# Optimization experiments

Hardware: AMD Instinct MI355X
Metric: run time of the kernel (lower is better)

The kernel has to match this reference:

```python
import jax, jax.numpy as jnp
import numpy as np

V = 4096          # vocab size (blank = V-1)
BLANK = V - 1
D = 512           # encoder dim
J = 640           # joint dim
E = 512           # embedding dim
H = 640           # prediction-net LSTM hidden
T = 8192          # frames


def setup_inputs() -> dict:
    key = jax.random.key(0)
    ks = jax.random.split(key, 12)
    s = lambda *sh: 1.0 / np.sqrt(sh[0])
    return {
        "enc_out": jax.random.normal(ks[0], (1, T, D), jnp.float32),
        "embed":   jax.random.normal(ks[1], (V, E), jnp.float32) * 0.02,
        "Wx":      jax.random.normal(ks[2], (E, 4 * H), jnp.float32) * s(E),
        "Wh":      jax.random.normal(ks[3], (H, 4 * H), jnp.float32) * s(H),
        "b_lstm":  jnp.zeros((4 * H,), jnp.float32),
        "Wdp":     jax.random.normal(ks[4], (H, J), jnp.float32) * s(H),
        "bdp":     jnp.zeros((J,), jnp.float32),
        "Wenc":    jax.random.normal(ks[5], (D, J), jnp.float32) * s(D),
        "benc":    jnp.zeros((J,), jnp.float32),
        "Wout":    jax.random.normal(ks[6], (J, V), jnp.float32) * s(J),
        "bout":    jnp.zeros((V,), jnp.float32),
    }


def _pred_step(tok, h, c, embed, Wx, Wh, b_lstm, Wdp, bdp):
    # single-token LSTM prediction-network step + output projection (decoder.pred)
    e = embed[tok]                                    # [E]
    g = e @ Wx + h @ Wh + b_lstm                      # [4H]
    i, f, gg, o = jnp.split(g, 4)
    c2 = jax.nn.sigmoid(f) * c + jax.nn.sigmoid(i) * jnp.tanh(gg)
    h2 = jax.nn.sigmoid(o) * jnp.tanh(c2)
    dp = h2 @ Wdp + bdp                               # [J] dec projection
    return dp, h2, c2


def reference(enc_out, embed, Wx, Wh, b_lstm, Wdp, bdp, Wenc, benc, Wout, bout):
    # decoder.enc_proj: [1,T,D] -> [T,J]
    enc_proj = enc_out[0] @ Wenc + benc

    # initial pred step fed with the blank token, zero hidden state
    dp0, h0, c0 = _pred_step(BLANK, jnp.zeros((H,), enc_out.dtype),
                             jnp.zeros((H,), enc_out.dtype),
                             embed, Wx, Wh, b_lstm, Wdp, bdp)

    def step(carry, enc_f):
        dp, h, c = carry
        # decoder.joint(enc, dec) = Wout @ tanh(enc_proj + dec_proj), then log_softmax
        logits = jnp.tanh(enc_f + dp) @ Wout + bout   # [V]
        logp = jax.nn.log_softmax(logits, axis=-1)
        tok = jnp.argmax(logp, axis=-1)
        dp2, h2, c2 = _pred_step(tok, h, c, embed, Wx, Wh, b_lstm, Wdp, bdp)
        nb = tok != BLANK                             # advance pred net only on emission
        carry = (jnp.where(nb, dp2, dp), jnp.where(nb, h2, h), jnp.where(nb, c2, c))
        return carry, logp

    _, logps = jax.lax.scan(step, (dp0, h0, c0), enc_proj)  # logps: [T, V]
    return logps
```

## Files before the change

kernel.cpp:

```cpp
#include <hip/hip_runtime.h>
#include <stdint.h>

#define T_FRAMES 8192
#define DIM_D 512
#define DIM_J 640
#define DIM_E 512
#define DIM_H 640
#define DIM_V 4096
#define G4H   2560
#define TOK_BLANK 4095
#define NBLK 256
#define NTHR 256

#define WS_HW   0
#define WS_DW   (WS_HW + 640*8)
#define WS_SA   (WS_DW + 640*8)
#define WS_SB   (WS_SA + 256*8)
#define WS_SC   (WS_SB + 256*8)
#define WS_BAR  (WS_SC + 256*8)

__device__ __forceinline__ float sigm(float x) { return 1.f / (1.f + __expf(-x)); }

__device__ __forceinline__ void st64(unsigned long long* p, unsigned tag, unsigned pay) {
  __hip_atomic_store(p, ((unsigned long long)tag << 32) | (unsigned long long)pay,
                     __ATOMIC_RELAXED, __HIP_MEMORY_SCOPE_AGENT);
}
__device__ __forceinline__ unsigned long long ld64(const unsigned long long* p) {
  return __hip_atomic_load(p, __ATOMIC_RELAXED, __HIP_MEMORY_SCOPE_AGENT);
}
__device__ __forceinline__ bool tagok(unsigned long long w, unsigned tag) {
  return (int)((unsigned)(w >> 32) - tag) >= 0;
}

__device__ __forceinline__ void gbar_init(unsigned* flags, int bid, int tid) {
  __syncthreads();
  if (tid == 0)
    __hip_atomic_store(&flags[bid * 16], 1u, __ATOMIC_RELEASE, __HIP_MEMORY_SCOPE_AGENT);
  unsigned f;
  do { f = __hip_atomic_load(&flags[tid * 16], __ATOMIC_RELAXED, __HIP_MEMORY_SCOPE_AGENT); }
  while ((int)(f - 1u) < 0);
  __builtin_amdgcn_fence(__ATOMIC_ACQUIRE, "agent");
  __syncthreads();
}

extern "C" __global__ void __launch_bounds__(NTHR, 1)
rnnt_greedy2(const float* __restrict__ enc,
             const float* __restrict__ embed,
             const float* __restrict__ Wx,
             const float* __restrict__ Wh,
             const float* __restrict__ b_lstm,
             const float* __restrict__ Wdp,
             const float* __restrict__ bdp,
             const float* __restrict__ Wenc,
             const float* __restrict__ benc,
             const float* __restrict__ Wout,
             const float* __restrict__ bout,
             float* __restrict__ out,
             unsigned long long* __restrict__ hw,
             unsigned long long* __restrict__ dw,
             unsigned long long* __restrict__ sA,
             unsigned long long* __restrict__ sB,
             unsigned long long* __restrict__ sC,
             unsigned* __restrict__ barflag)
{
  __shared__ float smem[29792];

  const int tid  = threadIdx.x;
  const int bid  = blockIdx.x;
  const int wid  = tid >> 6;
  const int lane = tid & 63;

  float* woutl = smem;
  float* wxl   = smem + 10240;
  float* whl   = smem + 16384;
  float* wdpl  = smem + 24064;
  float* h_com = smem + 25984;
  float* h2_l  = smem + 26624;
  float* dp_com= smem + 27264;
  float* x_l   = smem + 27904;
  float* enc_l = smem + 28544;
  float* ebuf  = smem + 29184;
  float* logit_l = smem + 29696;
  float* g_l     = smem + 29712;
  float* c_l     = smem + 29724;
  float* bout_l  = smem + 29728;
  float* blst_l  = smem + 29744;
  float* bdp_l   = smem + 29756;
  float* red     = smem + 29760;
  float* enc_lds = smem;

  const int h0 = (bid * 5) >> 1;
  const int h1 = ((bid + 1) * 5) >> 1;
  const int nH = h1 - h0;
  const int ncols = nH * 4;
  const int vb = bid << 4;

  {
    const int r0 = bid * 32;
    const float4* src = (const float4*)(enc + (size_t)r0 * DIM_D);
    float4* dst = (float4*)enc_lds;
    for (int i = tid; i < 32 * DIM_D / 4; i += NTHR) dst[i] = src[i];
    __syncthreads();
    for (int jj = tid; jj < DIM_J; jj += NTHR) {
      float acc[32];
      #pragma unroll
      for (int r = 0; r < 32; ++r) acc[r] = 0.f;
      for (int k = 0; k < DIM_D; ++k) {
        float w = Wenc[(size_t)k * DIM_J + jj];
        #pragma unroll
        for (int r = 0; r < 32; ++r) acc[r] += enc_lds[r * DIM_D + k] * w;
      }
      float bj = benc[jj];
      for (int r = 0; r < 32; ++r) out[(size_t)(r0 + r) * DIM_V + jj] = acc[r] + bj;
    }
    __syncthreads();
  }

  for (int idx = tid; idx < 16 * DIM_J; idx += NTHR) {
    int vl = idx / DIM_J, j = idx - vl * DIM_J;
    woutl[idx] = Wout[(size_t)j * DIM_V + vb + vl];
  }
  for (int idx = tid; idx < ncols * DIM_E; idx += NTHR) {
    int c = idx >> 9, k = idx & 511;
    int gcol = (c & 3) * DIM_H + h0 + (c >> 2);
    wxl[idx] = Wx[(size_t)k * G4H + gcol];
  }
  for (int idx = tid; idx < ncols * DIM_H; idx += NTHR) {
    int c = idx / DIM_H, k = idx - c * DIM_H;
    int gcol = (c & 3) * DIM_H + h0 + (c >> 2);
    whl[idx] = Wh[(size_t)k * G4H + gcol];
  }
  for (int idx = tid; idx < nH * DIM_H; idx += NTHR) {
    int jl = idx / DIM_H, k = idx - jl * DIM_H;
    wdpl[idx] = Wdp[(size_t)k * DIM_J + h0 + jl];
  }
  if (tid < 16) bout_l[tid] = bout[vb + tid];
  if (tid < ncols) blst_l[tid] = b_lstm[(tid & 3) * DIM_H + h0 + (tid >> 2)];
  if (tid < nH) bdp_l[tid] = bdp[h0 + tid];
  for (int i = tid; i < DIM_H; i += NTHR) h_com[i] = 0.f;
  if (tid < 4) c_l[tid] = 0.f;

  gbar_init(barflag, bid, tid);

  for (int t = -1; t < T_FRAMES; ++t) {
    const unsigned TAG = (unsigned)(t + 2);
    int tok; bool nb;

    if (t >= 0) {
      {
        const float* w0 = woutl + (wid * 4 + 0) * DIM_J;
        const float* w1 = woutl + (wid * 4 + 1) * DIM_J;
        const float* w2 = woutl + (wid * 4 + 2) * DIM_J;
        const float* w3 = woutl + (wid * 4 + 3) * DIM_J;
        float a0 = 0, a1 = 0, a2 = 0, a3 = 0;
        #pragma unroll
        for (int i = 0; i < 10; ++i) {
          int k = lane + (i << 6);
          float xv = x_l[k];
          a0 += xv * w0[k]; a1 += xv * w1[k]; a2 += xv * w2[k]; a3 += xv * w3[k];
        }
        #pragma unroll
        for (int m = 32; m; m >>= 1) {
          a0 += __shfl_xor(a0, m); a1 += __shfl_xor(a1, m);
          a2 += __shfl_xor(a2, m); a3 += __shfl_xor(a3, m);
        }
        if (lane == 0) {
          logit_l[wid * 4 + 0] = a0 + bout_l[wid * 4 + 0];
          logit_l[wid * 4 + 1] = a1 + bout_l[wid * 4 + 1];
          logit_l[wid * 4 + 2] = a2 + bout_l[wid * 4 + 2];
          logit_l[wid * 4 + 3] = a3 + bout_l[wid * 4 + 3];
        }
      }
      __syncthreads();

      {
        int prow = (t + 1 < T_FRAMES) ? t + 1 : t;
        if (tid >= 64 && tid < 224) {
          float4 ef = *(const float4*)(out + (size_t)prow * DIM_V + (tid - 64) * 4);
          *(float4*)(enc_l + (tid - 64) * 4) = ef;
        }
      }
      if (wid == 0) {
        float v  = (lane < 16) ? logit_l[lane] : -3.4e38f;
        int   vi = vb + (lane & 15);
        float m = v; int mi = vi;
        #pragma unroll
        for (int s = 32; s; s >>= 1) {
          float om = __shfl_xor(m, s); int oi = __shfl_xor(mi, s);
          if (om > m || (om == m && oi < mi)) { m = om; mi = oi; }
        }
        float e = (lane < 16) ? __expf(v - m) : 0.f;
        #pragma unroll
        for (int s = 32; s; s >>= 1) e += __shfl_xor(e, s);
        if (lane == 0) {
          st64(sA + bid, TAG, __float_as_uint(m));
          st64(sB + bid, TAG, __float_as_uint(e));
          st64(sC + bid, TAG, (unsigned)mi);
        }
      }

      unsigned long long wa = 0, wb = 0, wc = 0;
      {
        bool ra = false, rb = false, rc = false;
        while (!(ra && rb && rc)) {
          unsigned long long ta = wa, tb = wb, tc = wc;
          if (!ra) ta = ld64(sA + tid);
          if (!rb) tb = ld64(sB + tid);
          if (!rc) tc = ld64(sC + tid);
          if (!ra && tagok(ta, TAG)) { wa = ta; ra = true; }
          if (!rb && tagok(tb, TAG)) { wb = tb; rb = true; }
          if (!rc && tagok(tc, TAG)) { wc = tc; rc = true; }
          if (!(ra && rb && rc)) __builtin_amdgcn_s_sleep(1);
        }
      }
      const float mi0 = __uint_as_float((unsigned)wa);
      const float ei0 = __uint_as_float((unsigned)wb);
      const int   ii0 = (int)(unsigned)wc;
      float m = mi0; int idx = ii0;
      #pragma unroll
      for (int s = 32; s; s >>= 1) {
        float om = __shfl_xor(m, s); int oi = __shfl_xor(idx, s);
        if (om > m || (om == m && oi < idx)) { m = om; idx = oi; }
      }
      if (lane == 0) { red[wid] = m; ((int*)red)[4 + wid] = idx; }
      __syncthreads();
      float gm = red[0]; int gtok = ((int*)red)[4];
      #pragma unroll
      for (int w = 1; w < 4; ++w) {
        float om = red[w]; int oi = ((int*)red)[4 + w];
        if (om > gm || (om == gm && oi < gtok)) { gm = om; gtok = oi; }
      }
      float term = ei0 * __expf(mi0 - gm);
      #pragma unroll
      for (int s = 32; s; s >>= 1) term += __shfl_xor(term, s);
      if (lane == 0) red[8 + wid] = term;
      __syncthreads();
      const float lse = gm + __logf(red[8] + red[9] + red[10] + red[11]);

      if (tid < 16) out[(size_t)t * DIM_V + vb + tid] = logit_l[tid] - lse;

      tok = gtok;
      nb = (tok != TOK_BLANK);
      if (t == T_FRAMES - 1) break;
    } else {
      tok = TOK_BLANK;
      nb = true;
      if (tid >= 64 && tid < 224) {
        float4 ef = *(const float4*)(out + (size_t)(tid - 64) * 4);
        *(float4*)(enc_l + (tid - 64) * 4) = ef;
      }
    }

    if (tid < 128) {
      float4 ev = *(const float4*)(embed + (size_t)tok * DIM_E + tid * 4);
      *(float4*)(ebuf + tid * 4) = ev;
    }
    __syncthreads();
    for (int c = wid; c < ncols; c += 4) {
      const float* wx = wxl + c * DIM_E;
      const float* wh = whl + c * DIM_H;
      float acc = 0.f;
      #pragma unroll
      for (int i = 0; i < 8; ++i)  { int k = lane + (i << 6); acc += ebuf[k] * wx[k]; }
      #pragma unroll
      for (int i = 0; i < 10; ++i) { int k = lane + (i << 6); acc += h_com[k] * wh[k]; }
      #pragma unroll
      for (int s = 32; s; s >>= 1) acc += __shfl_xor(acc, s);
      if (lane == 0) g_l[c] = acc + blst_l[c];
    }
    __syncthreads();
    if (tid < nH) {
      float c_old = c_l[tid];
      float gi = g_l[tid * 4 + 0], gf = g_l[tid * 4 + 1];
      float gg = g_l[tid * 4 + 2], go_ = g_l[tid * 4 + 3];
      float c2  = sigm(gf) * c_old + sigm(gi) * tanhf(gg);
      float h2v = sigm(go_) * tanhf(c2);
      c_l[tid] = nb ? c2 : c_old;
      st64(hw + h0 + tid, TAG, __float_as_uint(h2v));
    }

    {
      const bool has2 = (tid < 128);
      unsigned long long w0 = 0, w1 = 0, w2 = 0;
      bool r0 = false, r1 = false, r2 = !has2;
      while (!(r0 && r1 && r2)) {
        unsigned long long t0 = w0, t1 = w1, t2 = w2;
        if (!r0) t0 = ld64(hw + tid);
        if (!r1) t1 = ld64(hw + tid + 256);
        if (!r2) t2 = ld64(hw + tid + 512);
        if (!r0 && tagok(t0, TAG)) { w0 = t0; r0 = true; }
        if (!r1 && tagok(t1, TAG)) { w1 = t1; r1 = true; }
        if (!r2 && tagok(t2, TAG)) { w2 = t2; r2 = true; }
        if (!(r0 && r1 && r2)) __builtin_amdgcn_s_sleep(1);
      }
      float h2a = __uint_as_float((unsigned)w0);
      float h2b = __uint_as_float((unsigned)w1);
      h2_l[tid] = h2a;        h_com[tid]       = nb ? h2a : h_com[tid];
      h2_l[tid + 256] = h2b;  h_com[tid + 256] = nb ? h2b : h_com[tid + 256];
      if (has2) {
        float h2c = __uint_as_float((unsigned)w2);
        h2_l[tid + 512] = h2c; h_com[tid + 512] = nb ? h2c : h_com[tid + 512];
      }
    }
    __syncthreads();

    if (wid < nH) {
      const float* wp = wdpl + wid * DIM_H;
      float acc = 0.f;
      #pragma unroll
      for (int i = 0; i < 10; ++i) { int k = lane + (i << 6); acc += h2_l[k] * wp[k]; }
      #pragma unroll
      for (int s = 32; s; s >>= 1) acc += __shfl_xor(acc, s);
      if (lane == 0) st64(dw + h0 + wid, TAG, __float_as_uint(acc + bdp_l[wid]));
    }

    {
      const bool has2 = (tid < 128);
      unsigned long long w0 = 0, w1 = 0, w2 = 0;
      bool r0 = false, r1 = false, r2 = !has2;
      while (!(r0 && r1 && r2)) {
        unsigned long long t0 = w0, t1 = w1, t2 = w2;
        if (!r0) t0 = ld64(dw + tid);
        if (!r1) t1 = ld64(dw + tid + 256);
        if (!r2) t2 = ld64(dw + tid + 512);
        if (!r0 && tagok(t0, TAG)) { w0 = t0; r0 = true; }
        if (!r1 && tagok(t1, TAG)) { w1 = t1; r1 = true; }
        if (!r2 && tagok(t2, TAG)) { w2 = t2; r2 = true; }
        if (!(r0 && r1 && r2)) __builtin_amdgcn_s_sleep(1);
      }
      float d0 = __uint_as_float((unsigned)w0);
      float d1 = __uint_as_float((unsigned)w1);
      float dn0 = nb ? d0 : dp_com[tid];
      float dn1 = nb ? d1 : dp_com[tid + 256];
      dp_com[tid] = dn0;       x_l[tid]       = tanhf(enc_l[tid] + dn0);
      dp_com[tid + 256] = dn1; x_l[tid + 256] = tanhf(enc_l[tid + 256] + dn1);
      if (has2) {
        float d2 = __uint_as_float((unsigned)w2);
        float dn2 = nb ? d2 : dp_com[tid + 512];
        dp_com[tid + 512] = dn2; x_l[tid + 512] = tanhf(enc_l[tid + 512] + dn2);
      }
    }
    __syncthreads();
  }
}

extern "C" void kernel_launch(void* const* d_in, const int* in_sizes, int n_in,
                              void* d_out, int out_size, void* d_ws, size_t ws_size,
                              hipStream_t stream) {
  const float* enc    = (const float*)d_in[0];
  const float* embed  = (const float*)d_in[1];
  const float* Wx     = (const float*)d_in[2];
  const float* Wh     = (const float*)d_in[3];
  const float* b_lstm = (const float*)d_in[4];
  const float* Wdp    = (const float*)d_in[5];
  const float* bdp    = (const float*)d_in[6];
  const float* Wenc   = (const float*)d_in[7];
  const float* benc   = (const float*)d_in[8];
  const float* Wout   = (const float*)d_in[9];
  const float* bout   = (const float*)d_in[10];
  float* out = (float*)d_out;
  char* ws = (char*)d_ws;
  unsigned long long* hw = (unsigned long long*)(ws + WS_HW);
  unsigned long long* dw = (unsigned long long*)(ws + WS_DW);
  unsigned long long* sA = (unsigned long long*)(ws + WS_SA);
  unsigned long long* sB = (unsigned long long*)(ws + WS_SB);
  unsigned long long* sC = (unsigned long long*)(ws + WS_SC);
  unsigned* barflag = (unsigned*)(ws + WS_BAR);

  hipLaunchKernelGGL(rnnt_greedy2, dim3(NBLK), dim3(NTHR), 0, stream,
                     enc, embed, Wx, Wh, b_lstm, Wdp, bdp, Wenc, benc, Wout, bout,
                     out, hw, dw, sA, sB, sC, barflag);
}
```

Before: 114.3 ms.

## Restructure per-frame cross-block exchange to cut global sync round-trips

Packs the per-block max and argmax into a single tagged 64-bit word and drops the third exchange array. The argmax is reduced by one wave so the token is known before the sum-exp exchange. The log-softmax normalisation moves off the critical path and overlaps the Wh part of the LSTM matvec, and each block now publishes tanh(enc+dp) directly instead of dp, so only one wave polls each exchange. The sum of exponentials is computed without subtracting the max, which risks overflow for large logits.

```diff
diff --git a/kernel.cpp b/kernel.cpp
--- a/kernel.cpp
+++ b/kernel.cpp
@@ -13,11 +13,10 @@
 #define NTHR 256
 
 #define WS_HW   0
-#define WS_DW   (WS_HW + 640*8)
-#define WS_SA   (WS_DW + 640*8)
+#define WS_XW   (WS_HW + 640*8)
+#define WS_SA   (WS_XW + 640*8)
 #define WS_SB   (WS_SA + 256*8)
-#define WS_SC   (WS_SB + 256*8)
-#define WS_BAR  (WS_SC + 256*8)
+#define WS_BAR  (WS_SB + 256*8)
 
 __device__ __forceinline__ float sigm(float x) { return 1.f / (1.f + __expf(-x)); }
 
@@ -30,6 +29,9 @@
 }
 __device__ __forceinline__ bool tagok(unsigned long long w, unsigned tag) {
   return (int)((unsigned)(w >> 32) - tag) >= 0;
+}
+__device__ __forceinline__ bool tagok16(unsigned long long w, unsigned tag16) {
+  return (short)((unsigned short)(w >> 48) - (unsigned short)tag16) >= 0;
 }
 
 __device__ __forceinline__ void gbar_init(unsigned* flags, int bid, int tid) {
@@ -44,7 +46,7 @@
 }
 
 extern "C" __global__ void __launch_bounds__(NTHR, 1)
-rnnt_greedy2(const float* __restrict__ enc,
+rnnt_greedy3(const float* __restrict__ enc,
              const float* __restrict__ embed,
              const float* __restrict__ Wx,
              const float* __restrict__ Wh,
@@ -57,13 +59,12 @@
              const float* __restrict__ bout,
              float* __restrict__ out,
              unsigned long long* __restrict__ hw,
-             unsigned long long* __restrict__ dw,
+             unsigned long long* __restrict__ xw,
              unsigned long long* __restrict__ sA,
              unsigned long long* __restrict__ sB,
-             unsigned long long* __restrict__ sC,
              unsigned* __restrict__ barflag)
 {
-  __shared__ float smem[29792];
+  __shared__ float smem[28512];
 
   const int tid  = threadIdx.x;
   const int bid  = blockIdx.x;
@@ -76,17 +77,16 @@
   float* wdpl  = smem + 24064;
   float* h_com = smem + 25984;
   float* h2_l  = smem + 26624;
-  float* dp_com= smem + 27264;
-  float* x_l   = smem + 27904;
-  float* enc_l = smem + 28544;
-  float* ebuf  = smem + 29184;
-  float* logit_l = smem + 29696;
-  float* g_l     = smem + 29712;
-  float* c_l     = smem + 29724;
-  float* bout_l  = smem + 29728;
-  float* blst_l  = smem + 29744;
-  float* bdp_l   = smem + 29756;
-  float* red     = smem + 29760;
+  float* x_l   = smem + 27264;
+  float* ebuf  = smem + 27904;
+  float* logit_l = smem + 28416;
+  float* g_l     = smem + 28432;
+  float* c_l     = smem + 28444;
+  float* dpc_l   = smem + 28448;
+  float* bout_l  = smem + 28452;
+  float* blst_l  = smem + 28468;
+  float* bdp_l   = smem + 28480;
+  float* red     = smem + 28484;
   float* enc_lds = smem;
 
   const int h0 = (bid * 5) >> 1;
@@ -142,10 +142,22 @@
 
   gbar_init(barflag, bid, tid);
 
+  const int  slot = (wid == 0) ? 0 : wid - 1;
+  const int  c0 = slot, c1 = slot + 3, c2 = slot + 6, c3 = slot + 9;
+  const bool v2 = (c2 < ncols), v3 = (c3 < ncols);
+  const bool lstmw = (wid != 1);
+
   for (int t = -1; t < T_FRAMES; ++t) {
     const unsigned TAG = (unsigned)(t + 2);
+    const bool last = (t == T_FRAMES - 1);
+
+    float encj = 0.f;
+    {
+      int prow = (t + 1 < T_FRAMES) ? (t + 1) : (T_FRAMES - 1);
+      if (wid < nH && lane == 0) encj = out[(size_t)prow * DIM_V + h0 + wid];
+    }
+
     int tok; bool nb;
-
     if (t >= 0) {
       {
         const float* w0 = woutl + (wid * 4 + 0) * DIM_J;
@@ -160,9 +172,9 @@
           a0 += xv * w0[k]; a1 += xv * w1[k]; a2 += xv * w2[k]; a3 += xv * w3[k];
         }
         #pragma unroll
-        for (int m = 32; m; m >>= 1) {
-          a0 += __shfl_xor(a0, m); a1 += __shfl_xor(a1, m);
-          a2 += __shfl_xor(a2, m); a3 += __shfl_xor(a3, m);
+        for (int s = 32; s; s >>= 1) {
+          a0 += __shfl_xor(a0, s); a1 += __shfl_xor(a1, s);
+          a2 += __shfl_xor(a2, s); a3 += __shfl_xor(a3, s);
         }
         if (lane == 0) {
           logit_l[wid * 4 + 0] = a0 + bout_l[wid * 4 + 0];
@@ -173,13 +185,6 @@
       }
       __syncthreads();
 
-      {
-        int prow = (t + 1 < T_FRAMES) ? t + 1 : t;
-        if (tid >= 64 && tid < 224) {
-          float4 ef = *(const float4*)(out + (size_t)prow * DIM_V + (tid - 64) * 4);
-          *(float4*)(enc_l + (tid - 64) * 4) = ef;
-        }
-      }
       if (wid == 0) {
         float v  = (lane < 16) ? logit_l[lane] : -3.4e38f;
         int   vi = vb + (lane & 15);
@@ -189,156 +194,171 @@
           float om = __shfl_xor(m, s); int oi = __shfl_xor(mi, s);
           if (om > m || (om == m && oi < mi)) { m = om; mi = oi; }
         }
-        float e = (lane < 16) ? __expf(v - m) : 0.f;
+        float e = (lane < 16) ? __expf(v) : 0.f;
         #pragma unroll
         for (int s = 32; s; s >>= 1) e += __shfl_xor(e, s);
         if (lane == 0) {
-          st64(sA + bid, TAG, __float_as_uint(m));
+          unsigned long long cw = ((unsigned long long)(TAG & 0xffffu) << 48)
+                                | ((unsigned long long)__float_as_uint(m) << 16)
+                                | (unsigned long long)(unsigned)(mi & 0xffff);
+          __hip_atomic_store(sA + bid, cw, __ATOMIC_RELAXED, __HIP_MEMORY_SCOPE_AGENT);
           st64(sB + bid, TAG, __float_as_uint(e));
-          st64(sC + bid, TAG, (unsigned)mi);
-        }
-      }
-
-      unsigned long long wa = 0, wb = 0, wc = 0;
-      {
-        bool ra = false, rb = false, rc = false;
-        while (!(ra && rb && rc)) {
-          unsigned long long ta = wa, tb = wb, tc = wc;
-          if (!ra) ta = ld64(sA + tid);
-          if (!rb) tb = ld64(sB + tid);
-          if (!rc) tc = ld64(sC + tid);
-          if (!ra && tagok(ta, TAG)) { wa = ta; ra = true; }
-          if (!rb && tagok(tb, TAG)) { wb = tb; rb = true; }
-          if (!rc && tagok(tc, TAG)) { wc = tc; rc = true; }
-          if (!(ra && rb && rc)) __builtin_amdgcn_s_sleep(1);
-        }
-      }
-      const float mi0 = __uint_as_float((unsigned)wa);
-      const float ei0 = __uint_as_float((unsigned)wb);
-      const int   ii0 = (int)(unsigned)wc;
-      float m = mi0; int idx = ii0;
+        }
+        unsigned long long cv0 = 0, cv1 = 0, cv2 = 0, cv3 = 0;
+        unsigned rdy = 0;
+        while (rdy != 0xfu) {
+          if (!(rdy & 1u)) { unsigned long long w = ld64(sA + lane);        if (tagok16(w, TAG)) { cv0 = w; rdy |= 1u; } }
+          if (!(rdy & 2u)) { unsigned long long w = ld64(sA + lane + 64);   if (tagok16(w, TAG)) { cv1 = w; rdy |= 2u; } }
+          if (!(rdy & 4u)) { unsigned long long w = ld64(sA + lane + 128);  if (tagok16(w, TAG)) { cv2 = w; rdy |= 4u; } }
+          if (!(rdy & 8u)) { unsigned long long w = ld64(sA + lane + 192);  if (tagok16(w, TAG)) { cv3 = w; rdy |= 8u; } }
+          if (rdy != 0xfu) __builtin_amdgcn_s_sleep(1);
+        }
+        float bm = -3.4e38f; int bi = 0x7fffffff;
+        {
+          float mm; int ii;
+          mm = __uint_as_float((unsigned)(cv0 >> 16)); ii = ((int)lane << 4)        | (int)(cv0 & 0xfu) | (int)((cv0 >> 4) & 0xff0u);
+          ii = (int)(cv0 & 0xffffu);
+          if (mm > bm || (mm == bm && ii < bi)) { bm = mm; bi = ii; }
+          mm = __uint_as_float((unsigned)(cv1 >> 16)); ii = (int)(cv1 & 0xffffu);
+          if (mm > bm || (mm == bm && ii < bi)) { bm = mm; bi = ii; }
+          mm = __uint_as_float((unsigned)(cv2 >> 16)); ii = (int)(cv2 & 0xffffu);
+          if (mm > bm || (mm == bm && ii < bi)) { bm = mm; bi = ii; }
+          mm = __uint_as_float((unsigned)(cv3 >> 16)); ii = (int)(cv3 & 0xffffu);
+          if (mm > bm || (mm == bm && ii < bi)) { bm = mm; bi = ii; }
+        }
+        #pragma unroll
+        for (int s = 32; s; s >>= 1) {
+          float om = __shfl_xor(bm, s); int oi = __shfl_xor(bi, s);
+          if (om > bm || (om == bm && oi < bi)) { bm = om; bi = oi; }
+        }
+        if (lane == 0) ((int*)red)[0] = bi;
+      }
+      __syncthreads();
+      tok = ((int*)red)[0];
+      nb = (tok != TOK_BLANK);
+    } else {
+      tok = TOK_BLANK; nb = true;
+    }
+
+    float4 ev;
+    if (wid >= 2 && !last) ev = *(const float4*)(embed + (size_t)tok * DIM_E + (tid - 128) * 4);
+    float acc0 = 0, acc1 = 0, acc2 = 0, acc3 = 0;
+    if (lstmw && !last) {
+      #pragma unroll
+      for (int i = 0; i < 10; ++i) {
+        int k = lane + (i << 6);
+        float hv = h_com[k];
+        acc0 += hv * whl[c0 * DIM_H + k];
+        acc1 += hv * whl[c1 * DIM_H + k];
+        if (v2) acc2 += hv * whl[c2 * DIM_H + k];
+        if (v3) acc3 += hv * whl[c3 * DIM_H + k];
+      }
+    }
+    if (wid == 1 && t >= 0) {
+      unsigned long long s0 = 0, s1 = 0, s2 = 0, s3 = 0;
+      unsigned rdy = 0;
+      while (rdy != 0xfu) {
+        if (!(rdy & 1u)) { unsigned long long w = ld64(sB + lane);        if (tagok(w, TAG)) { s0 = w; rdy |= 1u; } }
+        if (!(rdy & 2u)) { unsigned long long w = ld64(sB + lane + 64);   if (tagok(w, TAG)) { s1 = w; rdy |= 2u; } }
+        if (!(rdy & 4u)) { unsigned long long w = ld64(sB + lane + 128);  if (tagok(w, TAG)) { s2 = w; rdy |= 4u; } }
+        if (!(rdy & 8u)) { unsigned long long w = ld64(sB + lane + 192);  if (tagok(w, TAG)) { s3 = w; rdy |= 8u; } }
+        if (rdy != 0xfu) __builtin_amdgcn_s_sleep(1);
+      }
+      float s = __uint_as_float((unsigned)s0) + __uint_as_float((unsigned)s1)
+              + __uint_as_float((unsigned)s2) + __uint_as_float((unsigned)s3);
+      #pragma unroll
+      for (int sh = 32; sh; sh >>= 1) s += __shfl_xor(s, sh);
+      float lse = __logf(s);
+      if (lane < 16) out[(size_t)t * DIM_V + vb + lane] = logit_l[lane] - lse;
+    }
+    if (wid >= 2 && !last) *(float4*)(ebuf + (tid - 128) * 4) = ev;
+    __syncthreads();
+    if (last) break;
+
+    if (lstmw) {
+      #pragma unroll
+      for (int i = 0; i < 8; ++i) {
+        int k = lane + (i << 6);
+        float evv = ebuf[k];
+        acc0 += evv * wxl[c0 * DIM_E + k];
+        acc1 += evv * wxl[c1 * DIM_E + k];
+        if (v2) acc2 += evv * wxl[c2 * DIM_E + k];
+        if (v3) acc3 += evv * wxl[c3 * DIM_E + k];
+      }
       #pragma unroll
       for (int s = 32; s; s >>= 1) {
-        float om = __shfl_xor(m, s); int oi = __shfl_xor(idx, s);
-        if (om > m || (om == m && oi < idx)) { m = om; idx = oi; }
-      }
-      if (lane == 0) { red[wid] = m; ((int*)red)[4 + wid] = idx; }
-      __syncthreads();
-      float gm = red[0]; int gtok = ((int*)red)[4];
-      #pragma unroll
-      for (int w = 1; w < 4; ++w) {
-        float om = red[w]; int oi = ((int*)red)[4 + w];
-        if (om > gm || (om == gm && oi < gtok)) { gm = om; gtok = oi; }
-      }
-      float term = ei0 * __expf(mi0 - gm);
-      #pragma unroll
-      for (int s = 32; s; s >>= 1) term += __shfl_xor(term, s);
-      if (lane == 0) red[8 + wid] = term;
-      __syncthreads();
-      const float lse = gm + __logf(red[8] + red[9] + red[10] + red[11]);
-
-      if (tid < 16) out[(size_t)t * DIM_V + vb + tid] = logit_l[tid] - lse;
-
-      tok = gtok;
-      nb = (tok != TOK_BLANK);
-      if (t == T_FRAMES - 1) break;
-    } else {
-      tok = TOK_BLANK;
-      nb = true;
-      if (tid >= 64 && tid < 224) {
-        float4 ef = *(const float4*)(out + (size_t)(tid - 64) * 4);
-        *(float4*)(enc_l + (tid - 64) * 4) = ef;
-      }
-    }
-
-    if (tid < 128) {
-      float4 ev = *(const float4*)(embed + (size_t)tok * DIM_E + tid * 4);
-      *(float4*)(ebuf + tid * 4) = ev;
-    }
-    __syncthreads();
-    for (int c = wid; c < ncols; c += 4) {
-      const float* wx = wxl + c * DIM_E;
-      const float* wh = whl + c * DIM_H;
-      float acc = 0.f;
-      #pragma unroll
-      for (int i = 0; i < 8; ++i)  { int k = lane + (i << 6); acc += ebuf[k] * wx[k]; }
-      #pragma unroll
-      for (int i = 0; i < 10; ++i) { int k = lane + (i << 6); acc += h_com[k] * wh[k]; }
-      #pragma unroll
-      for (int s = 32; s; s >>= 1) acc += __shfl_xor(acc, s);
-      if (lane == 0) g_l[c] = acc + blst_l[c];
-    }
-    __syncthreads();
+        acc0 += __shfl_xor(acc0, s); acc1 += __shfl_xor(acc1, s);
+        acc2 += __shfl_xor(acc2, s); acc3 += __shfl_xor(acc3, s);
+      }
+      if (lane == 0) {
+        g_l[c0] = acc0 + blst_l[c0];
+        g_l[c1] = acc1 + blst_l[c1];
+        if (v2) g_l[c2] = acc2 + blst_l[c2];
+        if (v3) g_l[c3] = acc3 + blst_l[c3];
+      }
+    }
+    __syncthreads();
+
     if (tid < nH) {
       float c_old = c_l[tid];
       float gi = g_l[tid * 4 + 0], gf = g_l[tid * 4 + 1];
       float gg = g_l[tid * 4 + 2], go_ = g_l[tid * 4 + 3];
-      float c2  = sigm(gf) * c_old + sigm(gi) * tanhf(gg);
-      float h2v = sigm(go_) * tanhf(c2);
-      c_l[tid] = nb ? c2 : c_old;
+      float c2v = sigm(gf) * c_old + sigm(gi) * tanhf(gg);
+      float h2v = sigm(go_) * tanhf(c2v);
+      c_l[tid] = nb ? c2v : c_old;
       st64(hw + h0 + tid, TAG, __float_as_uint(h2v));
     }
-
-    {
-      const bool has2 = (tid < 128);
-      unsigned long long w0 = 0, w1 = 0, w2 = 0;
-      bool r0 = false, r1 = false, r2 = !has2;
-      while (!(r0 && r1 && r2)) {
-        unsigned long long t0 = w0, t1 = w1, t2 = w2;
-        if (!r0) t0 = ld64(hw + tid);
-        if (!r1) t1 = ld64(hw + tid + 256);
-        if (!r2) t2 = ld64(hw + tid + 512);
-        if (!r0 && tagok(t0, TAG)) { w0 = t0; r0 = true; }
-        if (!r1 && tagok(t1, TAG)) { w1 = t1; r1 = true; }
-        if (!r2 && tagok(t2, TAG)) { w2 = t2; r2 = true; }
-        if (!(r0 && r1 && r2)) __builtin_amdgcn_s_sleep(1);
-      }
-      float h2a = __uint_as_float((unsigned)w0);
-      float h2b = __uint_as_float((unsigned)w1);
-      h2_l[tid] = h2a;        h_com[tid]       = nb ? h2a : h_com[tid];
-      h2_l[tid + 256] = h2b;  h_com[tid + 256] = nb ? h2b : h_com[tid + 256];
-      if (has2) {
-        float h2c = __uint_as_float((unsigned)w2);
-        h2_l[tid + 512] = h2c; h_com[tid + 512] = nb ? h2c : h_com[tid + 512];
+    if (wid == 0) {
+      unsigned long long hv[10]; unsigned rdy = 0;
+      while (rdy != 0x3ffu) {
+        #pragma unroll
+        for (int i = 0; i < 10; ++i) {
+          if (!(rdy & (1u << i))) {
+            unsigned long long w = ld64(hw + lane + (i << 6));
+            if (tagok(w, TAG)) { hv[i] = w; rdy |= 1u << i; }
+          }
+        }
+        if (rdy != 0x3ffu) __builtin_amdgcn_s_sleep(1);
+      }
+      #pragma unroll
+      for (int i = 0; i < 10; ++i) {
+        int k = lane + (i << 6);
+        float h2v = __uint_as_float((unsigned)hv[i]);
+        h2_l[k] = h2v;
+        h_com[k] = nb ? h2v : h_com[k];
       }
     }
     __syncthreads();
 
     if (wid < nH) {
       const float* wp = wdpl + wid * DIM_H;
-      float acc = 0.f;
-      #pragma unroll
-      for (int i = 0; i < 10; ++i) { int k = lane + (i << 6); acc += h2_l[k] * wp[k]; }
-      #pragma unroll
-      for (int s = 32; s; s >>= 1) acc += __shfl_xor(acc, s);
-      if (lane == 0) st64(dw + h0 + wid, TAG, __float_as_uint(acc + bdp_l[wid]));
-    }
-
-    {
-      const bool has2 = (tid < 128);
-      unsigned long long w0 = 0, w1 = 0, w2 = 0;
-      bool r0 = false, r1 = false, r2 = !has2;
-      while (!(r0 && r1 && r2)) {
-        unsigned long long t0 = w0, t1 = w1, t2 = w2;
-        if (!r0) t0 = ld64(dw + tid);
-        if (!r1) t1 = ld64(dw + tid + 256);
-        if (!r2) t2 = ld64(dw + tid + 512);
-        if (!r0 && tagok(t0, TAG)) { w0 = t0; r0 = true; }
-        if (!r1 && tagok(t1, TAG)) { w1 = t1; r1 = true; }
-        if (!r2 && tagok(t2, TAG)) { w2 = t2; r2 = true; }
-        if (!(r0 && r1 && r2)) __builtin_amdgcn_s_sleep(1);
-      }
-      float d0 = __uint_as_float((unsigned)w0);
-      float d1 = __uint_as_float((unsigned)w1);
-      float dn0 = nb ? d0 : dp_com[tid];
-      float dn1 = nb ? d1 : dp_com[tid + 256];
-      dp_com[tid] = dn0;       x_l[tid]       = tanhf(enc_l[tid] + dn0);
-      dp_com[tid + 256] = dn1; x_l[tid + 256] = tanhf(enc_l[tid + 256] + dn1);
-      if (has2) {
-        float d2 = __uint_as_float((unsigned)w2);
-        float dn2 = nb ? d2 : dp_com[tid + 512];
-        dp_com[tid + 512] = dn2; x_l[tid + 512] = tanhf(enc_l[tid + 512] + dn2);
-      }
+      float a = 0.f;
+      #pragma unroll
+      for (int i = 0; i < 10; ++i) { int k = lane + (i << 6); a += h2_l[k] * wp[k]; }
+      #pragma unroll
+      for (int s = 32; s; s >>= 1) a += __shfl_xor(a, s);
+      if (lane == 0) {
+        float dp2 = a + bdp_l[wid];
+        float dpn = nb ? dp2 : dpc_l[wid];
+        dpc_l[wid] = dpn;
+        st64(xw + h0 + wid, TAG, __float_as_uint(tanhf(encj + dpn)));
+      }
+    }
+    if (wid == 0) {
+      unsigned long long xv[10]; unsigned rdy = 0;
+      while (rdy != 0x3ffu) {
+        #pragma unroll
+        for (int i = 0; i < 10; ++i) {
+          if (!(rdy & (1u << i))) {
+            unsigned long long w = ld64(xw + lane + (i << 6));
+            if (tagok(w, TAG)) { xv[i] = w; rdy |= 1u << i; }
+          }
+        }
+        if (rdy != 0x3ffu) __builtin_amdgcn_s_sleep(1);
+      }
+      #pragma unroll
+      for (int i = 0; i < 10; ++i)
+        x_l[lane + (i << 6)] = __uint_as_float((unsigned)xv[i]);
     }
     __syncthreads();
   }
@@ -361,13 +381,12 @@
   float* out = (float*)d_out;
   char* ws = (char*)d_ws;
   unsigned long long* hw = (unsigned long long*)(ws + WS_HW);
-  unsigned long long* dw = (unsigned long long*)(ws + WS_DW);
+  unsigned long long* xw = (unsigned long long*)(ws + WS_XW);
   unsigned long long* sA = (unsigned long long*)(ws + WS_SA);
   unsigned long long* sB = (unsigned long long*)(ws + WS_SB);
-  unsigned long long* sC = (unsigned long long*)(ws + WS_SC);
   unsigned* barflag = (unsigned*)(ws + WS_BAR);
 
-  hipLaunchKernelGGL(rnnt_greedy2, dim3(NBLK), dim3(NTHR), 0, stream,
+  hipLaunchKernelGGL(rnnt_greedy3, dim3(NBLK), dim3(NTHR), 0, stream,
                      enc, embed, Wx, Wh, b_lstm, Wdp, bdp, Wenc, benc, Wout, bout,
-                     out, hw, dw, sA, sB, sC, barflag);
-}
+                     out, hw, xw, sA, sB, barflag);
+}
```

Measured after the change: 129.4 ms. 13.3% more time.
